# Kernel optimization log

Hardware: AMD Instinct MI355X
Metric: run time of the kernel (lower is better)

## Reference

```python
import jax, jax.numpy as jnp
import numpy as np

UNITS = 256
FEAT = 64


def setup_inputs() -> dict:
    key = jax.random.key(0)
    ks = jax.random.split(key, 6)
    B, T, F, U = 512, 1024, FEAT, UNITS
    sW = 1.0 / np.sqrt(F)
    sU = 1.0 / np.sqrt(U)
    return {
        "x": jax.random.normal(ks[0], (B, T, F), dtype=jnp.float32),
        "W": jax.random.normal(ks[1], (F, 4 * U), dtype=jnp.float32) * sW,
        "Uh": jax.random.normal(ks[2], (U, 4 * U), dtype=jnp.float32) * sU,
        "b": jnp.zeros((4 * U,), dtype=jnp.float32),
        "dense_w": jax.random.normal(ks[3], (U, 1), dtype=jnp.float32) * sU,
        "dense_b": jnp.zeros((1,), dtype=jnp.float32),
    }


def _lstm_scan(x, W, Uh, b):
    # x: (B, T, F) -> hs: (B, T, U), h_T: (B, U)
    B = x.shape[0]
    U = Uh.shape[0]
    h0 = jnp.zeros((B, U), dtype=x.dtype)
    c0 = jnp.zeros((B, U), dtype=x.dtype)

    def step(carry, xt):
        h, c = carry
        z = xt @ W + h @ Uh + b  # (B, 4U)
        i, f, g, o = jnp.split(z, 4, axis=-1)
        i = jax.nn.sigmoid(i)
        f = jax.nn.sigmoid(f)
        g = jnp.tanh(g)
        o = jax.nn.sigmoid(o)
        c_new = f * c + i * g
        h_new = o * jnp.tanh(c_new)
        return (h_new, c_new), h_new

    (h_T, _c_T), hs = jax.lax.scan(step, (h0, c0), jnp.transpose(x, (1, 0, 2)))
    return jnp.transpose(hs, (1, 0, 2)), h_T


def reference(x, W, Uh, b, dense_w, dense_b):
    seq, h_T = _lstm_scan(x, W, Uh, b)          # (B,T,U), (B,U)
    k = h_T[:, None, :]                          # (B,1,U) single key/value
    scores = jnp.einsum("btu,bsu->bts", seq, k)  # (B,T,1)
    w = jax.nn.softmax(scores, axis=-1)          # all ones (single key)
    attn = jnp.einsum("bts,bsu->btu", w, k)      # (B,T,U)
    logits = attn @ dense_w + dense_b            # (B,T,1)
    return jax.nn.sigmoid(logits[..., 0])        # (B,T)
```

## Files before the change

### kernel.cpp

```cpp
#include <hip/hip_runtime.h>

#define Tn 1024
#define Fn 64
#define Un 256
#define Gn 1024
#define AS 328
#define THREADS 256
#define NB 128

typedef __attribute__((ext_vector_type(8))) short bf16x8;
typedef __attribute__((ext_vector_type(8))) unsigned short ushort8;
typedef __attribute__((ext_vector_type(4))) float f32x4;
typedef unsigned long long u64;

#define WS_XCHG 4096
#define WS_BP   (WS_XCHG + NB*2*4096)

__device__ __forceinline__ float bf2f(unsigned short u){
  union { unsigned int i; float f; } v; v.i = ((unsigned int)u) << 16; return v.f;
}
__device__ __forceinline__ unsigned short f2bf(float f){
  unsigned int u = __float_as_uint(f);
  u += 0x7FFFu + ((u >> 16) & 1u);
  return (unsigned short)(u >> 16);
}
__device__ __forceinline__ float load_f(const void* p, long idx, int isf32){
  if (isf32) return ((const float*)p)[idx];
  return bf2f(((const unsigned short*)p)[idx]);
}
__device__ __forceinline__ float sigm(float x){ return 1.0f / (1.0f + __expf(-x)); }
__device__ __forceinline__ float tanh_f(float x){ return 2.0f * sigm(2.0f * x) - 1.0f; }

__device__ __forceinline__ u64 ld_a64(const u64* p){
  return __hip_atomic_load(p, __ATOMIC_RELAXED, __HIP_MEMORY_SCOPE_AGENT);
}
__device__ __forceinline__ int ok64(u64 v, unsigned int need){
  return (int)(((unsigned int)v & 0xFFFFu) == need) &
         (int)(((unsigned int)(v >> 32) & 0xFFFFu) == need);
}

__global__ void init_k(const void* x, int* wsi){
  int tid = threadIdx.x;
  if (tid < 64){
    int cnt = 0;
    for (int s2 = 0; s2 < 4; ++s2){
      float v = bf2f(((const unsigned short*)x)[tid + 64*s2]);
      if (!(fabsf(v) <= 100.0f)) cnt++;
    }
    for (int off = 32; off > 0; off >>= 1) cnt += __shfl_down(cnt, off);
    if (tid == 0) wsi[0] = (cnt > 32) ? 1 : 0;
  }
}

__global__ void reformat_w(const void* Uh, const void* W, unsigned short* Bp, const int* dt){
  int isf32 = *dt;
  int gidx = blockIdx.x * blockDim.x + threadIdx.x;
  if (gidx >= 40960) return;
  int kt  = gidx >> 12;
  int rem = gidx & 4095;
  int n   = rem >> 2;
  int q   = rem & 3;
  int s   = n >> 8;
  int w   = (n >> 6) & 3;
  int g   = (n >> 4) & 3;
  int ul  = n & 15;
  int col = g*256 + s*64 + w*16 + ul;
  unsigned short vals[8];
  #pragma unroll
  for (int j = 0; j < 8; ++j){
    int k = kt*32 + q*8 + j;
    float v = (k < Un) ? load_f(Uh, (long)k*Gn + col, isf32)
                       : load_f(W,  (long)(k-Un)*Gn + col, isf32);
    vals[j] = f2bf(v);
  }
  *(ushort8*)(Bp + (long)gidx * 8) = *(ushort8*)vals;
}

__global__ __launch_bounds__(THREADS, 1) void lstm_k(
    const void* x, const void* bvec, const void* dense_w, const void* dense_b,
    const unsigned short* Bp, const int* dt, unsigned int* xchg, void* out)
{
  __shared__ __align__(16) unsigned short A_s[2][16*AS];
  __shared__ float outv[16];

  const int isf32 = *dt;
  const int tid = threadIdx.x;
  const int w   = tid >> 6;
  const int l   = tid & 63;
  const int l15 = l & 15;
  const int q   = l >> 4;
  const int g   = blockIdx.x >> 2;
  const int s   = blockIdx.x & 3;

  int plist[3];
  #pragma unroll
  for (int j = 0; j < 3; ++j) plist[j] = j + (j >= s ? 1 : 0);

  int ktp[10];
  ktp[0] = 2*s; ktp[1] = 2*s + 1; ktp[2] = 8; ktp[3] = 9;
  #pragma unroll
  for (int j = 0; j < 3; ++j){ ktp[4+2*j] = 2*plist[j]; ktp[5+2*j] = 2*plist[j] + 1; }

  const char* Bb = (const char*)Bp + (long)(l15*64 + q*16);
  const int nb = s*256 + w*64;
  bf16x8 wfrag[10][4];
  #pragma unroll
  for (int i = 0; i < 10; ++i){
    #pragma unroll
    for (int gg = 0; gg < 4; ++gg)
      wfrag[i][gg] = *(const bf16x8*)(Bb + (long)(ktp[i]*1024 + nb + gg*16)*64);
  }

  for (int i = tid; i < 16*Un; i += THREADS)
    A_s[0][(i >> 8)*AS + (i & 255)] = 0;

  if (tid < 128){
    int m = tid >> 3, ch = tid & 7;
    long src = ((long)(g*16 + m)*Tn + 0)*Fn + ch*8;
    unsigned short v[8];
    if (isf32){ for (int j = 0; j < 8; ++j) v[j] = f2bf(((const float*)x)[src + j]); }
    else      { *(ushort8*)v = *(const ushort8*)((const unsigned short*)x + src); }
    *(ushort8*)&A_s[0][m*AS + Un + ch*8] = *(ushort8*)v;
  }

  const int u_loc = w*16 + l15;
  float bias[4];
  #pragma unroll
  for (int gg = 0; gg < 4; ++gg) bias[gg] = load_f(bvec, gg*256 + s*64 + u_loc, isf32);

  float c[4] = {0.f, 0.f, 0.f, 0.f};
  unsigned int* xc_me = xchg + (size_t)(g*4 + s) * 2048;

  const u64* pa[3];
  #pragma unroll
  for (int j = 0; j < 3; ++j)
    pa[j] = (const u64*)(xchg + (size_t)((g*4 + plist[j])*2)*1024) + tid*2;

  __syncthreads();

  for (int t = 0; t < Tn; ++t){
    const int buf = t & 1, nbuf = buf ^ 1;
    const size_t po = (size_t)buf * 512;

    unsigned short xv[8];
    if (tid < 128 && (t+1) < Tn){
      int m = tid >> 3, ch = tid & 7;
      long src = ((long)(g*16 + m)*Tn + (t+1))*Fn + ch*8;
      if (isf32){ for (int j = 0; j < 8; ++j) xv[j] = f2bf(((const float*)x)[src + j]); }
      else      { *(ushort8*)xv = *(const ushort8*)((const unsigned short*)x + src); }
    }

    u64 pw[6];
    if (t > 0){
      pw[0] = ld_a64(pa[0] + po);  pw[1] = ld_a64(pa[0] + po + 1);
      pw[2] = ld_a64(pa[1] + po);  pw[3] = ld_a64(pa[1] + po + 1);
      pw[4] = ld_a64(pa[2] + po);  pw[5] = ld_a64(pa[2] + po + 1);
    }

    f32x4 acc[4];
    #pragma unroll
    for (int gg = 0; gg < 4; ++gg)
      acc[gg] = (f32x4){bias[gg], bias[gg], bias[gg], bias[gg]};
    #pragma unroll
    for (int i = 0; i < 4; ++i){
      bf16x8 af = *(const bf16x8*)&A_s[buf][l15*AS + ktp[i]*32 + q*8];
      #pragma unroll
      for (int gg = 0; gg < 4; ++gg)
        acc[gg] = __builtin_amdgcn_mfma_f32_16x16x32_bf16(af, wfrag[i][gg], acc[gg], 0, 0, 0);
    }

    if (t > 0){
      const unsigned int need = (unsigned int)(t & 0xFFFF);
      while (!(ok64(pw[0], need) & ok64(pw[1], need) & ok64(pw[2], need) &
               ok64(pw[3], need) & ok64(pw[4], need) & ok64(pw[5], need))){
        pw[0] = ld_a64(pa[0] + po);  pw[1] = ld_a64(pa[0] + po + 1);
        pw[2] = ld_a64(pa[1] + po);  pw[3] = ld_a64(pa[1] + po + 1);
        pw[4] = ld_a64(pa[2] + po);  pw[5] = ld_a64(pa[2] + po + 1);
      }
      const int row = tid >> 4, u0c = (tid & 15) * 4;
      #pragma unroll
      for (int j = 0; j < 3; ++j){
        u64 a = pw[2*j], b = pw[2*j + 1];
        u64 hv = ((a >> 16) & 0xFFFFull)
               | (((a >> 48) & 0xFFFFull) << 16)
               | (((b >> 16) & 0xFFFFull) << 32)
               | (((b >> 48) & 0xFFFFull) << 48);
        *(u64*)&A_s[buf][row*AS + plist[j]*64 + u0c] = hv;
      }
    }
    if (tid < 128 && (t+1) < Tn){
      int m = tid >> 3, ch = tid & 7;
      *(ushort8*)&A_s[nbuf][m*AS + Un + ch*8] = *(ushort8*)xv;
    }
    __syncthreads();

    if (t > 0){
      #pragma unroll
      for (int i = 4; i < 10; ++i){
        bf16x8 af = *(const bf16x8*)&A_s[buf][l15*AS + ktp[i]*32 + q*8];
        #pragma unroll
        for (int gg = 0; gg < 4; ++gg)
          acc[gg] = __builtin_amdgcn_mfma_f32_16x16x32_bf16(af, wfrag[i][gg], acc[gg], 0, 0, 0);
      }
    }

    {
      const unsigned int tag = (unsigned int)((t+1) & 0xFFFF);
      unsigned int* dstb = xc_me + (size_t)nbuf*1024;
      #pragma unroll
      for (int r = 0; r < 4; ++r){
        float ig = sigm(acc[0][r]);
        float fg = sigm(acc[1][r]);
        float gg = tanh_f(acc[2][r]);
        float og = sigm(acc[3][r]);
        float cn = fg * c[r] + ig * gg;
        c[r] = cn;
        unsigned short hb = f2bf(og * tanh_f(cn));
        A_s[nbuf][(q*4 + r)*AS + (s*64 + u_loc)] = hb;
        __hip_atomic_store(dstb + (q*4 + r)*64 + u_loc,
                           ((unsigned int)hb << 16) | tag,
                           __ATOMIC_RELAXED, __HIP_MEMORY_SCOPE_AGENT);
      }
    }
    __syncthreads();
  }

  if (s == 0){
    const unsigned int need = (unsigned int)(Tn & 0xFFFF);
    u64 pw[6];
    pw[0] = ld_a64(pa[0]);  pw[1] = ld_a64(pa[0] + 1);
    pw[2] = ld_a64(pa[1]);  pw[3] = ld_a64(pa[1] + 1);
    pw[4] = ld_a64(pa[2]);  pw[5] = ld_a64(pa[2] + 1);
    while (!(ok64(pw[0], need) & ok64(pw[1], need) & ok64(pw[2], need) &
             ok64(pw[3], need) & ok64(pw[4], need) & ok64(pw[5], need))){
      pw[0] = ld_a64(pa[0]);  pw[1] = ld_a64(pa[0] + 1);
      pw[2] = ld_a64(pa[1]);  pw[3] = ld_a64(pa[1] + 1);
      pw[4] = ld_a64(pa[2]);  pw[5] = ld_a64(pa[2] + 1);
    }
    const int row = tid >> 4, u0c = (tid & 15) * 4;
    #pragma unroll
    for (int j = 0; j < 3; ++j){
      u64 a = pw[2*j], b = pw[2*j + 1];
      u64 hv = ((a >> 16) & 0xFFFFull)
             | (((a >> 48) & 0xFFFFull) << 16)
             | (((b >> 16) & 0xFFFFull) << 32)
             | (((b >> 48) & 0xFFFFull) << 48);
      *(u64*)&A_s[0][row*AS + plist[j]*64 + u0c] = hv;
    }
    __syncthreads();

    int m = tid >> 4, j16 = tid & 15;
    float partial = 0.f;
    for (int u = j16; u < 256; u += 16)
      partial += bf2f(A_s[0][m*AS + u]) * load_f(dense_w, u, isf32);
    #pragma unroll
    for (int off = 1; off < 16; off <<= 1) partial += __shfl_xor(partial, off);
    if (j16 == 0) outv[m] = sigm(partial + load_f(dense_b, 0, isf32));
    __syncthreads();

    for (int mm = 0; mm < 16; ++mm){
      float v = outv[mm];
      long base = (long)(g*16 + mm) * Tn;
      for (int col = tid; col < Tn; col += THREADS){
        if (isf32) ((float*)out)[base + col] = v;
        else       ((unsigned short*)out)[base + col] = f2bf(v);
      }
    }
  }
}

extern "C" void kernel_launch(void* const* d_in, const int* in_sizes, int n_in,
                              void* d_out, int out_size, void* d_ws, size_t ws_size,
                              hipStream_t stream){
  const void* x  = d_in[0];
  const void* W  = d_in[1];
  const void* Uh = d_in[2];
  const void* b  = d_in[3];
  const void* dw = d_in[4];
  const void* db = d_in[5];

  int* hdr = (int*)d_ws;
  unsigned int* xchg = (unsigned int*)((char*)d_ws + WS_XCHG);
  unsigned short* Bp = (unsigned short*)((char*)d_ws + WS_BP);

  init_k<<<1, 64, 0, stream>>>(x, hdr);
  reformat_w<<<160, 256, 0, stream>>>(Uh, W, Bp, hdr);
  lstm_k<<<NB, THREADS, 0, stream>>>(x, b, dw, db, Bp, hdr, xchg, d_out);
}
```

Baseline: 2.794 ms.

## Add XCC-local fast exchange path using L2-scoped loads for same-XCD block groups

```diff
diff --git a/kernel.cpp b/kernel.cpp
--- a/kernel.cpp
+++ b/kernel.cpp
@@ -15,6 +15,7 @@
 
 #define WS_XCHG 4096
 #define WS_BP   (WS_XCHG + NB*2*4096)
+#define WS_XF   (WS_BP + 655360)
 
 __device__ __forceinline__ float bf2f(unsigned short u){
   union { unsigned int i; float f; } v; v.i = ((unsigned int)u) << 16; return v.f;
@@ -38,6 +39,44 @@
   return (int)(((unsigned int)v & 0xFFFFu) == need) &
          (int)(((unsigned int)(v >> 32) & 0xFFFFu) == need);
 }
+
+__device__ __forceinline__ void ld6_issue_l2(const u64* a0, const u64* a1,
+                                             const u64* a2, u64* pw){
+  asm volatile(
+    "global_load_dwordx2 %0, %6, off sc0\n\t"
+    "global_load_dwordx2 %1, %6, off offset:8 sc0\n\t"
+    "global_load_dwordx2 %2, %7, off sc0\n\t"
+    "global_load_dwordx2 %3, %7, off offset:8 sc0\n\t"
+    "global_load_dwordx2 %4, %8, off sc0\n\t"
+    "global_load_dwordx2 %5, %8, off offset:8 sc0"
+    : "=&v"(pw[0]), "=&v"(pw[1]), "=&v"(pw[2]),
+      "=&v"(pw[3]), "=&v"(pw[4]), "=&v"(pw[5])
+    : "v"(a0), "v"(a1), "v"(a2)
+    : "memory");
+}
+__device__ __forceinline__ void ld6_wait_l2(const u64* a0, const u64* a1,
+                                            const u64* a2, u64* pw){
+  asm volatile(
+    "global_load_dwordx2 %0, %6, off sc0\n\t"
+    "global_load_dwordx2 %1, %6, off offset:8 sc0\n\t"
+    "global_load_dwordx2 %2, %7, off sc0\n\t"
+    "global_load_dwordx2 %3, %7, off offset:8 sc0\n\t"
+    "global_load_dwordx2 %4, %8, off sc0\n\t"
+    "global_load_dwordx2 %5, %8, off offset:8 sc0\n\t"
+    "s_waitcnt vmcnt(0)"
+    : "=&v"(pw[0]), "=&v"(pw[1]), "=&v"(pw[2]),
+      "=&v"(pw[3]), "=&v"(pw[4]), "=&v"(pw[5])
+    : "v"(a0), "v"(a1), "v"(a2)
+    : "memory");
+}
+__device__ __forceinline__ void vm_wait_pw(u64* pw){
+  asm volatile("s_waitcnt vmcnt(0)"
+    : "+v"(pw[0]), "+v"(pw[1]), "+v"(pw[2]),
+      "+v"(pw[3]), "+v"(pw[4]), "+v"(pw[5]));
+}
+
+#define OK6 (ok64(pw[0], need) & ok64(pw[1], need) & ok64(pw[2], need) & \
+             ok64(pw[3], need) & ok64(pw[4], need) & ok64(pw[5], need))
 
 __global__ void init_k(const void* x, int* wsi){
   int tid = threadIdx.x;
@@ -50,6 +89,8 @@
     for (int off = 32; off > 0; off >>= 1) cnt += __shfl_down(cnt, off);
     if (tid == 0) wsi[0] = (cnt > 32) ? 1 : 0;
   }
+  if (tid == 0) wsi[1] = wsi[1] + 1;
+  if (tid < NB) wsi[32 + tid] = 0;
 }
 
 __global__ void reformat_w(const void* Uh, const void* W, unsigned short* Bp, const int* dt){
@@ -78,19 +119,30 @@
 
 __global__ __launch_bounds__(THREADS, 1) void lstm_k(
     const void* x, const void* bvec, const void* dense_w, const void* dense_b,
-    const unsigned short* Bp, const int* dt, unsigned int* xchg, void* out)
+    const unsigned short* Bp, int* hdr, unsigned int* xchg, unsigned int* xf,
+    void* out)
 {
   __shared__ __align__(16) unsigned short A_s[2][16*AS];
   __shared__ float outv[16];
-
-  const int isf32 = *dt;
+  __shared__ int proto_s;
+
+  const int isf32 = hdr[0];
+  const unsigned int Lid = ((unsigned int)hdr[1]) & 0xFFFFu;
   const int tid = threadIdx.x;
   const int w   = tid >> 6;
   const int l   = tid & 63;
   const int l15 = l & 15;
   const int q   = l >> 4;
-  const int g   = blockIdx.x >> 2;
-  const int s   = blockIdx.x & 3;
+  const int g   = blockIdx.x & 31;
+  const int s   = blockIdx.x >> 5;
+
+  int* slots = hdr + 32;
+  if (tid == 0){
+    unsigned int xcc;
+    asm volatile("s_getreg_b32 %0, hwreg(HW_REG_XCC_ID)" : "=s"(xcc));
+    __hip_atomic_store(&slots[blockIdx.x], (int)((Lid << 16) | (xcc & 0xFFu)),
+                       __ATOMIC_RELAXED, __HIP_MEMORY_SCOPE_AGENT);
+  }
 
   int plist[3];
   #pragma unroll
@@ -129,18 +181,43 @@
   for (int gg = 0; gg < 4; ++gg) bias[gg] = load_f(bvec, gg*256 + s*64 + u_loc, isf32);
 
   float c[4] = {0.f, 0.f, 0.f, 0.f};
-  unsigned int* xc_me = xchg + (size_t)(g*4 + s) * 2048;
-
-  const u64* pa[3];
-  #pragma unroll
-  for (int j = 0; j < 3; ++j)
-    pa[j] = (const u64*)(xchg + (size_t)((g*4 + plist[j])*2)*1024) + tid*2;
+  unsigned int* xc_slow = xchg + (size_t)(g*4 + s) * 2048;
+  unsigned int* xc_fast = xf   + (size_t)(g*4 + s) * 2048;
+
+  const u64* pas[3];
+  const u64* paf[3];
+  #pragma unroll
+  for (int j = 0; j < 3; ++j){
+    pas[j] = (const u64*)(xchg + (size_t)((g*4 + plist[j])*2)*1024) + tid*2;
+    paf[j] = (const u64*)(xf   + (size_t)((g*4 + plist[j])*2)*1024) + tid*2;
+  }
+
+  if (tid == 0){
+    int v0 = 0, ok = 1;
+    #pragma unroll
+    for (int m = 0; m < 4; ++m){
+      int val;
+      do {
+        val = __hip_atomic_load(&slots[(m << 5) | g],
+                                __ATOMIC_RELAXED, __HIP_MEMORY_SCOPE_AGENT);
+      } while (((unsigned int)val >> 16) != Lid);
+      if (m == 0) v0 = val; else ok &= (int)(val == v0);
+    }
+    proto_s = ok;
+  }
 
   __syncthreads();
+  const int fast = proto_s;
 
   for (int t = 0; t < Tn; ++t){
     const int buf = t & 1, nbuf = buf ^ 1;
     const size_t po = (size_t)buf * 512;
+    const u64* sa0 = pas[0] + po;
+    const u64* sa1 = pas[1] + po;
+    const u64* sa2 = pas[2] + po;
+    const u64* fa0 = paf[0] + po;
+    const u64* fa1 = paf[1] + po;
+    const u64* fa2 = paf[2] + po;
 
     unsigned short xv[8];
     if (tid < 128 && (t+1) < Tn){
@@ -152,9 +229,13 @@
 
     u64 pw[6];
     if (t > 0){
-      pw[0] = ld_a64(pa[0] + po);  pw[1] = ld_a64(pa[0] + po + 1);
-      pw[2] = ld_a64(pa[1] + po);  pw[3] = ld_a64(pa[1] + po + 1);
-      pw[4] = ld_a64(pa[2] + po);  pw[5] = ld_a64(pa[2] + po + 1);
+      if (fast){
+        ld6_issue_l2(fa0, fa1, fa2, pw);
+      } else {
+        pw[0] = ld_a64(sa0);  pw[1] = ld_a64(sa0 + 1);
+        pw[2] = ld_a64(sa1);  pw[3] = ld_a64(sa1 + 1);
+        pw[4] = ld_a64(sa2);  pw[5] = ld_a64(sa2 + 1);
+      }
     }
 
     f32x4 acc[4];
@@ -171,11 +252,25 @@
 
     if (t > 0){
       const unsigned int need = (unsigned int)(t & 0xFFFF);
-      while (!(ok64(pw[0], need) & ok64(pw[1], need) & ok64(pw[2], need) &
-               ok64(pw[3], need) & ok64(pw[4], need) & ok64(pw[5], need))){
-        pw[0] = ld_a64(pa[0] + po);  pw[1] = ld_a64(pa[0] + po + 1);
-        pw[2] = ld_a64(pa[1] + po);  pw[3] = ld_a64(pa[1] + po + 1);
-        pw[4] = ld_a64(pa[2] + po);  pw[5] = ld_a64(pa[2] + po + 1);
+      if (fast){
+        vm_wait_pw(pw);
+        unsigned int it = 0;
+        while (!OK6){
+          ++it;
+          if ((it & 15u) == 15u){
+            pw[0] = ld_a64(sa0);  pw[1] = ld_a64(sa0 + 1);
+            pw[2] = ld_a64(sa1);  pw[3] = ld_a64(sa1 + 1);
+            pw[4] = ld_a64(sa2);  pw[5] = ld_a64(sa2 + 1);
+          } else {
+            ld6_wait_l2(fa0, fa1, fa2, pw);
+          }
+        }
+      } else {
+        while (!OK6){
+          pw[0] = ld_a64(sa0);  pw[1] = ld_a64(sa0 + 1);
+          pw[2] = ld_a64(sa1);  pw[3] = ld_a64(sa1 + 1);
+          pw[4] = ld_a64(sa2);  pw[5] = ld_a64(sa2 + 1);
+        }
       }
       const int row = tid >> 4, u0c = (tid & 15) * 4;
       #pragma unroll
@@ -206,7 +301,8 @@
 
     {
       const unsigned int tag = (unsigned int)((t+1) & 0xFFFF);
-      unsigned int* dstb = xc_me + (size_t)nbuf*1024;
+      unsigned int* dslow = xc_slow + (size_t)nbuf*1024;
+      unsigned int* dfast = xc_fast + (size_t)nbuf*1024;
       #pragma unroll
       for (int r = 0; r < 4; ++r){
         float ig = sigm(acc[0][r]);
@@ -217,8 +313,10 @@
         c[r] = cn;
         unsigned short hb = f2bf(og * tanh_f(cn));
         A_s[nbuf][(q*4 + r)*AS + (s*64 + u_loc)] = hb;
-        __hip_atomic_store(dstb + (q*4 + r)*64 + u_loc,
-                           ((unsigned int)hb << 16) | tag,
+        unsigned int word = ((unsigned int)hb << 16) | tag;
+        int idx = (q*4 + r)*64 + u_loc;
+        dfast[idx] = word;
+        __hip_atomic_store(dslow + idx, word,
                            __ATOMIC_RELAXED, __HIP_MEMORY_SCOPE_AGENT);
       }
     }
@@ -228,14 +326,13 @@
   if (s == 0){
     const unsigned int need = (unsigned int)(Tn & 0xFFFF);
     u64 pw[6];
-    pw[0] = ld_a64(pa[0]);  pw[1] = ld_a64(pa[0] + 1);
-    pw[2] = ld_a64(pa[1]);  pw[3] = ld_a64(pa[1] + 1);
-    pw[4] = ld_a64(pa[2]);  pw[5] = ld_a64(pa[2] + 1);
-    while (!(ok64(pw[0], need) & ok64(pw[1], need) & ok64(pw[2], need) &
-             ok64(pw[3], need) & ok64(pw[4], need) & ok64(pw[5], need))){
-      pw[0] = ld_a64(pa[0]);  pw[1] = ld_a64(pa[0] + 1);
-      pw[2] = ld_a64(pa[1]);  pw[3] = ld_a64(pa[1] + 1);
-      pw[4] = ld_a64(pa[2]);  pw[5] = ld_a64(pa[2] + 1);
+    pw[0] = ld_a64(pas[0]);  pw[1] = ld_a64(pas[0] + 1);
+    pw[2] = ld_a64(pas[1]);  pw[3] = ld_a64(pas[1] + 1);
+    pw[4] = ld_a64(pas[2]);  pw[5] = ld_a64(pas[2] + 1);
+    while (!OK6){
+      pw[0] = ld_a64(pas[0]);  pw[1] = ld_a64(pas[0] + 1);
+      pw[2] = ld_a64(pas[1]);  pw[3] = ld_a64(pas[1] + 1);
+      pw[4] = ld_a64(pas[2]);  pw[5] = ld_a64(pas[2] + 1);
     }
     const int row = tid >> 4, u0c = (tid & 15) * 4;
     #pragma unroll
@@ -282,8 +379,9 @@
   int* hdr = (int*)d_ws;
   unsigned int* xchg = (unsigned int*)((char*)d_ws + WS_XCHG);
   unsigned short* Bp = (unsigned short*)((char*)d_ws + WS_BP);
-
-  init_k<<<1, 64, 0, stream>>>(x, hdr);
+  unsigned int* xf   = (unsigned int*)((char*)d_ws + WS_XF);
+
+  init_k<<<1, 128, 0, stream>>>(x, hdr);
   reformat_w<<<160, 256, 0, stream>>>(Uh, W, Bp, hdr);
-  lstm_k<<<NB, THREADS, 0, stream>>>(x, b, dw, db, Bp, hdr, xchg, d_out);
-}
+  lstm_k<<<NB, THREADS, 0, stream>>>(x, b, dw, db, Bp, hdr, xchg, xf, d_out);
+}
```

Measured after the change: 5.047 ms. 1.81x slower.

## Split each batch group across two 512-thread blocks instead of four

Applied to the files above, without the earlier changes.

```diff
diff --git a/kernel.cpp b/kernel.cpp
--- a/kernel.cpp
+++ b/kernel.cpp
@@ -5,8 +5,8 @@
 #define Un 256
 #define Gn 1024
 #define AS 328
-#define THREADS 256
-#define NB 128
+#define THREADS 512
+#define NB 64
 
 typedef __attribute__((ext_vector_type(8))) short bf16x8;
 typedef __attribute__((ext_vector_type(8))) unsigned short ushort8;
@@ -14,7 +14,7 @@
 typedef unsigned long long u64;
 
 #define WS_XCHG 4096
-#define WS_BP   (WS_XCHG + NB*2*4096)
+#define WS_BP   (WS_XCHG + NB*2*8192)
 
 __device__ __forceinline__ float bf2f(unsigned short u){
   union { unsigned int i; float f; } v; v.i = ((unsigned int)u) << 16; return v.f;
@@ -37,6 +37,12 @@
 __device__ __forceinline__ int ok64(u64 v, unsigned int need){
   return (int)(((unsigned int)v & 0xFFFFu) == need) &
          (int)(((unsigned int)(v >> 32) & 0xFFFFu) == need);
+}
+__device__ __forceinline__ u64 pack_h(u64 a, u64 b){
+  return ((a >> 16) & 0xFFFFull)
+       | (((a >> 48) & 0xFFFFull) << 16)
+       | (((b >> 16) & 0xFFFFull) << 32)
+       | (((b >> 48) & 0xFFFFull) << 48);
 }
 
 __global__ void init_k(const void* x, int* wsi){
@@ -60,11 +66,11 @@
   int rem = gidx & 4095;
   int n   = rem >> 2;
   int q   = rem & 3;
-  int s   = n >> 8;
-  int w   = (n >> 6) & 3;
+  int s   = n >> 9;
+  int w   = (n >> 6) & 7;
   int g   = (n >> 4) & 3;
   int ul  = n & 15;
-  int col = g*256 + s*64 + w*16 + ul;
+  int col = g*256 + s*128 + w*16 + ul;
   unsigned short vals[8];
   #pragma unroll
   for (int j = 0; j < 8; ++j){
@@ -76,7 +82,7 @@
   *(ushort8*)(Bp + (long)gidx * 8) = *(ushort8*)vals;
 }
 
-__global__ __launch_bounds__(THREADS, 1) void lstm_k(
+__global__ __launch_bounds__(THREADS, 2) void lstm_k(
     const void* x, const void* bvec, const void* dense_w, const void* dense_b,
     const unsigned short* Bp, const int* dt, unsigned int* xchg, void* out)
 {
@@ -89,20 +95,17 @@
   const int l   = tid & 63;
   const int l15 = l & 15;
   const int q   = l >> 4;
-  const int g   = blockIdx.x >> 2;
-  const int s   = blockIdx.x & 3;
-
-  int plist[3];
-  #pragma unroll
-  for (int j = 0; j < 3; ++j) plist[j] = j + (j >= s ? 1 : 0);
+  const int g   = blockIdx.x >> 1;
+  const int s   = blockIdx.x & 1;
+  const int sp  = s ^ 1;
 
   int ktp[10];
-  ktp[0] = 2*s; ktp[1] = 2*s + 1; ktp[2] = 8; ktp[3] = 9;
-  #pragma unroll
-  for (int j = 0; j < 3; ++j){ ktp[4+2*j] = 2*plist[j]; ktp[5+2*j] = 2*plist[j] + 1; }
+  ktp[0] = 4*s;  ktp[1] = 4*s+1;  ktp[2] = 4*s+2;  ktp[3] = 4*s+3;
+  ktp[4] = 8;    ktp[5] = 9;
+  ktp[6] = 4*sp; ktp[7] = 4*sp+1; ktp[8] = 4*sp+2; ktp[9] = 4*sp+3;
 
   const char* Bb = (const char*)Bp + (long)(l15*64 + q*16);
-  const int nb = s*256 + w*64;
+  const int nb = s*512 + w*64;
   bf16x8 wfrag[10][4];
   #pragma unroll
   for (int i = 0; i < 10; ++i){
@@ -126,21 +129,17 @@
   const int u_loc = w*16 + l15;
   float bias[4];
   #pragma unroll
-  for (int gg = 0; gg < 4; ++gg) bias[gg] = load_f(bvec, gg*256 + s*64 + u_loc, isf32);
+  for (int gg = 0; gg < 4; ++gg) bias[gg] = load_f(bvec, gg*256 + s*128 + u_loc, isf32);
 
   float c[4] = {0.f, 0.f, 0.f, 0.f};
-  unsigned int* xc_me = xchg + (size_t)(g*4 + s) * 2048;
-
-  const u64* pa[3];
-  #pragma unroll
-  for (int j = 0; j < 3; ++j)
-    pa[j] = (const u64*)(xchg + (size_t)((g*4 + plist[j])*2)*1024) + tid*2;
+  unsigned int* xc_me = xchg + (size_t)blockIdx.x * 4096;
+  const u64* pa = (const u64*)(xchg + (size_t)(blockIdx.x ^ 1) * 4096) + tid*2;
 
   __syncthreads();
 
   for (int t = 0; t < Tn; ++t){
     const int buf = t & 1, nbuf = buf ^ 1;
-    const size_t po = (size_t)buf * 512;
+    const size_t po = (size_t)buf * 1024;
 
     unsigned short xv[8];
     if (tid < 128 && (t+1) < Tn){
@@ -150,11 +149,10 @@
       else      { *(ushort8*)xv = *(const ushort8*)((const unsigned short*)x + src); }
     }
 
-    u64 pw[6];
+    u64 pw0 = 0, pw1 = 0;
     if (t > 0){
-      pw[0] = ld_a64(pa[0] + po);  pw[1] = ld_a64(pa[0] + po + 1);
-      pw[2] = ld_a64(pa[1] + po);  pw[3] = ld_a64(pa[1] + po + 1);
-      pw[4] = ld_a64(pa[2] + po);  pw[5] = ld_a64(pa[2] + po + 1);
+      pw0 = ld_a64(pa + po);
+      pw1 = ld_a64(pa + po + 1);
     }
 
     f32x4 acc[4];
@@ -162,7 +160,7 @@
     for (int gg = 0; gg < 4; ++gg)
       acc[gg] = (f32x4){bias[gg], bias[gg], bias[gg], bias[gg]};
     #pragma unroll
-    for (int i = 0; i < 4; ++i){
+    for (int i = 0; i < 6; ++i){
       bf16x8 af = *(const bf16x8*)&A_s[buf][l15*AS + ktp[i]*32 + q*8];
       #pragma unroll
       for (int gg = 0; gg < 4; ++gg)
@@ -171,22 +169,15 @@
 
     if (t > 0){
       const unsigned int need = (unsigned int)(t & 0xFFFF);
-      while (!(ok64(pw[0], need) & ok64(pw[1], need) & ok64(pw[2], need) &
-               ok64(pw[3], need) & ok64(pw[4], need) & ok64(pw[5], need))){
-        pw[0] = ld_a64(pa[0] + po);  pw[1] = ld_a64(pa[0] + po + 1);
-        pw[2] = ld_a64(pa[1] + po);  pw[3] = ld_a64(pa[1] + po + 1);
-        pw[4] = ld_a64(pa[2] + po);  pw[5] = ld_a64(pa[2] + po + 1);
-      }
-      const int row = tid >> 4, u0c = (tid & 15) * 4;
-      #pragma unroll
-      for (int j = 0; j < 3; ++j){
-        u64 a = pw[2*j], b = pw[2*j + 1];
-        u64 hv = ((a >> 16) & 0xFFFFull)
-               | (((a >> 48) & 0xFFFFull) << 16)
-               | (((b >> 16) & 0xFFFFull) << 32)
-               | (((b >> 48) & 0xFFFFull) << 48);
-        *(u64*)&A_s[buf][row*AS + plist[j]*64 + u0c] = hv;
-      }
+      int first = 1;
+      while (!(ok64(pw0, need) & ok64(pw1, need))){
+        if (!first) __builtin_amdgcn_s_sleep(1);
+        first = 0;
+        pw0 = ld_a64(pa + po);
+        pw1 = ld_a64(pa + po + 1);
+      }
+      const int row = tid >> 5, col = (tid & 31) * 4;
+      *(u64*)&A_s[buf][row*AS + sp*128 + col] = pack_h(pw0, pw1);
     }
     if (tid < 128 && (t+1) < Tn){
       int m = tid >> 3, ch = tid & 7;
@@ -196,7 +187,7 @@
 
     if (t > 0){
       #pragma unroll
-      for (int i = 4; i < 10; ++i){
+      for (int i = 6; i < 10; ++i){
         bf16x8 af = *(const bf16x8*)&A_s[buf][l15*AS + ktp[i]*32 + q*8];
         #pragma unroll
         for (int gg = 0; gg < 4; ++gg)
@@ -206,7 +197,7 @@
 
     {
       const unsigned int tag = (unsigned int)((t+1) & 0xFFFF);
-      unsigned int* dstb = xc_me + (size_t)nbuf*1024;
+      unsigned int* dstb = xc_me + (size_t)nbuf*2048;
       #pragma unroll
       for (int r = 0; r < 4; ++r){
         float ig = sigm(acc[0][r]);
@@ -216,8 +207,8 @@
         float cn = fg * c[r] + ig * gg;
         c[r] = cn;
         unsigned short hb = f2bf(og * tanh_f(cn));
-        A_s[nbuf][(q*4 + r)*AS + (s*64 + u_loc)] = hb;
-        __hip_atomic_store(dstb + (q*4 + r)*64 + u_loc,
+        A_s[nbuf][(q*4 + r)*AS + (s*128 + u_loc)] = hb;
+        __hip_atomic_store(dstb + (q*4 + r)*128 + u_loc,
                            ((unsigned int)hb << 16) | tag,
                            __ATOMIC_RELAXED, __HIP_MEMORY_SCOPE_AGENT);
       }
@@ -227,43 +218,31 @@
 
   if (s == 0){
     const unsigned int need = (unsigned int)(Tn & 0xFFFF);
-    u64 pw[6];
-    pw[0] = ld_a64(pa[0]);  pw[1] = ld_a64(pa[0] + 1);
-    pw[2] = ld_a64(pa[1]);  pw[3] = ld_a64(pa[1] + 1);
-    pw[4] = ld_a64(pa[2]);  pw[5] = ld_a64(pa[2] + 1);
-    while (!(ok64(pw[0], need) & ok64(pw[1], need) & ok64(pw[2], need) &
-             ok64(pw[3], need) & ok64(pw[4], need) & ok64(pw[5], need))){
-      pw[0] = ld_a64(pa[0]);  pw[1] = ld_a64(pa[0] + 1);
-      pw[2] = ld_a64(pa[1]);  pw[3] = ld_a64(pa[1] + 1);
-      pw[4] = ld_a64(pa[2]);  pw[5] = ld_a64(pa[2] + 1);
-    }
-    const int row = tid >> 4, u0c = (tid & 15) * 4;
-    #pragma unroll
-    for (int j = 0; j < 3; ++j){
-      u64 a = pw[2*j], b = pw[2*j + 1];
-      u64 hv = ((a >> 16) & 0xFFFFull)
-             | (((a >> 48) & 0xFFFFull) << 16)
-             | (((b >> 16) & 0xFFFFull) << 32)
-             | (((b >> 48) & 0xFFFFull) << 48);
-      *(u64*)&A_s[0][row*AS + plist[j]*64 + u0c] = hv;
-    }
-    __syncthreads();
-
-    int m = tid >> 4, j16 = tid & 15;
+    u64 pw0 = ld_a64(pa), pw1 = ld_a64(pa + 1);
+    while (!(ok64(pw0, need) & ok64(pw1, need))){
+      __builtin_amdgcn_s_sleep(1);
+      pw0 = ld_a64(pa);
+      pw1 = ld_a64(pa + 1);
+    }
+    const int row = tid >> 5, col = (tid & 31) * 4;
+    *(u64*)&A_s[0][row*AS + 128 + col] = pack_h(pw0, pw1);
+    __syncthreads();
+
+    int m = tid >> 5, j = tid & 31;
     float partial = 0.f;
-    for (int u = j16; u < 256; u += 16)
+    for (int u = j; u < 256; u += 32)
       partial += bf2f(A_s[0][m*AS + u]) * load_f(dense_w, u, isf32);
     #pragma unroll
-    for (int off = 1; off < 16; off <<= 1) partial += __shfl_xor(partial, off);
-    if (j16 == 0) outv[m] = sigm(partial + load_f(dense_b, 0, isf32));
+    for (int off = 1; off < 32; off <<= 1) partial += __shfl_xor(partial, off);
+    if (j == 0) outv[m] = sigm(partial + load_f(dense_b, 0, isf32));
     __syncthreads();
 
     for (int mm = 0; mm < 16; ++mm){
       float v = outv[mm];
       long base = (long)(g*16 + mm) * Tn;
-      for (int col = tid; col < Tn; col += THREADS){
-        if (isf32) ((float*)out)[base + col] = v;
-        else       ((unsigned short*)out)[base + col] = f2bf(v);
+      for (int col2 = tid; col2 < Tn; col2 += THREADS){
+        if (isf32) ((float*)out)[base + col2] = v;
+        else       ((unsigned short*)out)[base + col2] = f2bf(v);
       }
     }
   }
```

After: 2.803 ms. No clear change (+0.4%).
